# Performance work log

Measured on AMD Instinct MI355X. Metric: run time of the kernel, lower is better.

## Reference

```python
import jax, jax.numpy as jnp
import numpy as np
from jax import lax

EPS = 1e-5
NBIT = 127.0  # 8-bit symmetric: 2^(8-1)-1

def ste_round(x):
    return x + lax.stop_gradient(jnp.round(x) - x)

def quant_act(x, rng_max):
    # symmetric fake-quant of activations with learned per-cluster range
    s = rng_max / NBIT
    xq = jnp.clip(ste_round(x / s), -NBIT, NBIT) * s
    return xq, s

def fold_bn(w, gamma, beta, mean, var):
    std = jnp.sqrt(var + EPS)
    scale = gamma / std
    w_f = w * scale[:, None, None, None]
    b_f = beta - mean * scale
    return w_f, b_f

def quant_weight(w):
    # per-output-channel symmetric quant
    s = jnp.max(jnp.abs(w), axis=(1, 2, 3), keepdims=True) / NBIT
    wq = jnp.clip(ste_round(w / s), -NBIT, NBIT) * s
    return wq, s.reshape(-1)

def conv(x, w, stride=1, groups=1, pad=0):
    return lax.conv_general_dilated(
        x, w, window_strides=(stride, stride),
        padding=((pad, pad), (pad, pad)),
        dimension_numbers=('NCHW', 'OIHW', 'NCHW'),
        feature_group_count=groups)

def setup_inputs() -> dict:
    key = jax.random.key(0)
    ks = jax.random.split(key, 24)
    B, Cin, H, W = 64, 96, 28, 28
    Cmid, Cout, NC = 576, 96, 4
    d = {}
    d['x'] = jax.random.normal(ks[0], (B, Cin, H, W), dtype=jnp.float32)
    # conv1: 1x1 expansion
    d['w1'] = jax.random.normal(ks[1], (Cmid, Cin, 1, 1), jnp.float32) * 0.1
    d['g1'] = jax.random.uniform(ks[2], (Cmid,), minval=0.5, maxval=1.5)
    d['b1'] = jax.random.normal(ks[3], (Cmid,)) * 0.1
    d['m1'] = jax.random.normal(ks[4], (Cmid,)) * 0.1
    d['v1'] = jax.random.uniform(ks[5], (Cmid,), minval=0.5, maxval=1.5)
    # conv2: 3x3 depthwise
    d['w2'] = jax.random.normal(ks[6], (Cmid, 1, 3, 3), jnp.float32) * 0.1
    d['g2'] = jax.random.uniform(ks[7], (Cmid,), minval=0.5, maxval=1.5)
    d['b2'] = jax.random.normal(ks[8], (Cmid,)) * 0.1
    d['m2'] = jax.random.normal(ks[9], (Cmid,)) * 0.1
    d['v2'] = jax.random.uniform(ks[10], (Cmid,), minval=0.5, maxval=1.5)
    # conv3: 1x1 projection
    d['w3'] = jax.random.normal(ks[11], (Cout, Cmid, 1, 1), jnp.float32) * 0.1
    d['g3'] = jax.random.uniform(ks[12], (Cout,), minval=0.5, maxval=1.5)
    d['b3'] = jax.random.normal(ks[13], (Cout,)) * 0.1
    d['m3'] = jax.random.normal(ks[14], (Cout,)) * 0.1
    d['v3'] = jax.random.uniform(ks[15], (Cout,), minval=0.5, maxval=1.5)
    # per-cluster learned activation ranges for the 4 QuantAct modules
    d['r0'] = jax.random.uniform(ks[16], (NC,), minval=2.0, maxval=8.0)
    d['r1'] = jax.random.uniform(ks[17], (NC,), minval=2.0, maxval=8.0)
    d['r2'] = jax.random.uniform(ks[18], (NC,), minval=2.0, maxval=8.0)
    d['r3'] = jax.random.uniform(ks[19], (NC,), minval=2.0, maxval=8.0)
    d['cluster'] = 2
    return d

def reference(x, w1, g1, b1, m1, v1, w2, g2, b2, m2, v2,
              w3, g3, b3, m3, v3, r0, r1, r2, r3, cluster):
    identity = x  # residual path (in==out, stride==1)
    # QuantAct -> conv1 (BN-folded, per-channel quant) -> ReLU6
    xq, s0 = quant_act(x, r0[cluster])
    w1f, bf1 = fold_bn(w1, g1, b1, m1, v1)
    w1q, ws1 = quant_weight(w1f)
    y = conv(xq, w1q) + bf1[None, :, None, None]
    y = jnp.clip(y, 0.0, 6.0)
    # QuantAct1 -> depthwise conv2 -> ReLU6
    yq, s1 = quant_act(y, r1[cluster])
    w2f, bf2 = fold_bn(w2, g2, b2, m2, v2)
    w2q, ws2 = quant_weight(w2f)
    y = conv(yq, w2q, stride=1, groups=w2.shape[0], pad=1) + bf2[None, :, None, None]
    y = jnp.clip(y, 0.0, 6.0)
    # QuantAct2 -> conv3 projection
    yq, s2 = quant_act(y, r2[cluster])
    w3f, bf3 = fold_bn(w3, g3, b3, m3, v3)
    w3q, ws3 = quant_weight(w3f)
    y = conv(yq, w3q) + bf3[None, :, None, None]
    # residual add, then int32 requant
    y = y + identity
    out, s3 = quant_act(y, r3[cluster])
    return out, s3
```

## Files before the change

### kernel.cpp

```cpp
#include <hip/hip_runtime.h>
#include <cstdint>
#include <cstddef>

typedef int   v4i __attribute__((ext_vector_type(4)));
typedef float v4f __attribute__((ext_vector_type(4)));
typedef unsigned int u32;

constexpr int B_   = 64;
constexpr int CIN  = 96;
constexpr int P_   = 784;
constexpr int CMID = 576;
constexpr int COUT = 96;
constexpr int NOUT = B_ * COUT * P_;
constexpr float NBITF = 127.0f;
constexpr float EPSF  = 1e-5f;
constexpr float MAGICF = 12582912.0f;
constexpr int   BIASI  = 0x4B400000;

constexpr int Y1S = 43;

__device__ __forceinline__ int dot3(u32 a, u32 w, int acc) {
#if __has_builtin(__builtin_amdgcn_sdot4)
    return __builtin_amdgcn_sdot4((int)a, (int)w, acc, false);
#else
    return acc + (int)(signed char)(a)        * (int)(signed char)(w)
               + (int)(signed char)(a >> 8)   * (int)(signed char)(w >> 8)
               + (int)(signed char)(a >> 16)  * (int)(signed char)(w >> 16);
#endif
}

__device__ __forceinline__ void tr4(u32 S0, u32 S1, u32 S2, u32 S3, u32 O[4]) {
    u32 u01 = __builtin_amdgcn_perm(S1, S0, 0x05010400u);
    u32 u23 = __builtin_amdgcn_perm(S3, S2, 0x05010400u);
    u32 v01 = __builtin_amdgcn_perm(S1, S0, 0x07030602u);
    u32 v23 = __builtin_amdgcn_perm(S3, S2, 0x07030602u);
    O[0] = __builtin_amdgcn_perm(u23, u01, 0x05040100u);
    O[1] = __builtin_amdgcn_perm(u23, u01, 0x07060302u);
    O[2] = __builtin_amdgcn_perm(v23, v01, 0x05040100u);
    O[3] = __builtin_amdgcn_perm(v23, v01, 0x07060302u);
}

__device__ __forceinline__ u32 pack4(u32 t0, u32 t1, u32 t2, u32 t3) {
    u32 p01 = __builtin_amdgcn_perm(t1, t0, 0x05010400u);
    u32 p23 = __builtin_amdgcn_perm(t3, t2, 0x05010400u);
    return __builtin_amdgcn_perm(p23, p01, 0x05040100u);
}

__global__ __launch_bounds__(256)
void prep_w(const float* __restrict__ w1, const float* __restrict__ g1,
            const float* __restrict__ b1, const float* __restrict__ m1,
            const float* __restrict__ v1,
            const float* __restrict__ w2, const float* __restrict__ g2,
            const float* __restrict__ b2, const float* __restrict__ m2,
            const float* __restrict__ v2,
            const float* __restrict__ w3, const float* __restrict__ g3,
            const float* __restrict__ b3, const float* __restrict__ m3,
            const float* __restrict__ v3,
            const float* __restrict__ r0, const float* __restrict__ r1,
            const float* __restrict__ r2, const int* __restrict__ cluster,
            int8_t* __restrict__ w1qp, float2* __restrict__ e1,
            v4i* __restrict__ w2pk,    float2* __restrict__ e2,
            int8_t* __restrict__ w3qp, float2* __restrict__ e3)
{
    int tid = threadIdx.x;
    int c = cluster[0];
    int lane = tid & 63, wv = tid >> 6;
    int blk = blockIdx.x * 4 + wv;

    const float *w, *g, *bb, *mm, *vv;
    int oc, K, which;
    if (blk < CMID)            { which = 0; w = w1; g = g1; bb = b1; mm = m1; vv = v1; oc = blk;            K = CIN;  }
    else if (blk < 2 * CMID)   { which = 1; w = w2; g = g2; bb = b2; mm = m2; vv = v2; oc = blk - CMID;     K = 9;    }
    else                       { which = 2; w = w3; g = g3; bb = b3; mm = m3; vv = v3; oc = blk - 2 * CMID; K = CMID; }

    float scale = g[oc] / sqrtf(vv[oc] + EPSF);

    float mx = 0.f;
    for (int k = lane; k < K; k += 64)
        mx = fmaxf(mx, fabsf(w[oc * K + k] * scale));
    #pragma unroll
    for (int off = 1; off < 64; off <<= 1)
        mx = fmaxf(mx, __shfl_xor(mx, off));

    float s = mx / NBITF;

    int myq = 0;
    for (int k = lane; k < K; k += 64) {
        float wf = w[oc * K + k] * scale;
        float q  = fminf(fmaxf(rintf(wf / s), -127.f), 127.f);
        if (which == 0)      w1qp[oc * 144 + k] = (int8_t)q;
        else if (which == 1) myq = (int)q;
        else                 w3qp[oc * 592 + k] = (int8_t)q;
    }
    if (which == 0 && lane < 12)
        ((u32*)(w1qp + oc * 144))[24 + lane] = 0u;
    if (which == 1) {
        u32 qq[9];
        #pragma unroll
        for (int t = 0; t < 9; t++) qq[t] = (u32)__shfl(myq, t, 64) & 0xffu;
        if (lane == 0) {
            v4i pk;
            pk[0] = (int)(qq[0] | (qq[1] << 8) | (qq[2] << 16));
            pk[1] = (int)(qq[3] | (qq[4] << 8) | (qq[5] << 16));
            pk[2] = (int)(qq[6] | (qq[7] << 8) | (qq[8] << 16));
            pk[3] = 0;
            w2pk[oc] = pk;
        }
    }
    if (lane == 0) {
        float bf = bb[oc] - mm[oc] * scale;
        float s0 = r0[c] / NBITF, s1 = r1[c] / NBITF, s2 = r2[c] / NBITF;
        if (which == 0) {
            float inv_s1 = NBITF / r1[c];
            e1[oc] = make_float2(s0 * s * inv_s1, bf * inv_s1);
        } else if (which == 1) {
            float inv_s2 = NBITF / r2[c];
            e2[oc] = make_float2(s1 * s * inv_s2, bf * inv_s2);
        } else {
            e3[oc] = make_float2(s2 * s, bf);
        }
    }
}

__global__ __launch_bounds__(256, 2)
void conv123d(const v4i* __restrict__ w1q4,
              const float2* __restrict__ e1,
              const v4i* __restrict__ w2pk, const float2* __restrict__ e2,
              const int8_t* __restrict__ w3qp, const float2* __restrict__ e3,
              const float* __restrict__ x,
              const float* __restrict__ r0,
              const float* __restrict__ r1, const float* __restrict__ r2,
              const float* __restrict__ r3, const int* __restrict__ cluster,
              float* __restrict__ out)
{
    __shared__ v4i xw[11 * 6 * 16];
    __shared__ u32 y1s[4][48 * Y1S];
    __shared__ v4i y2c[12 * 112];

    int tid = threadIdx.x, b = blockIdx.y, rt = blockIdx.x;
    int R0 = 4 * rt;
    int W0 = (R0 - 1) * 28;
    int lane = tid & 63, wv = tid >> 6;
    int n = lane & 15, q4 = lane >> 4;

    int   c      = cluster[0];
    float inv_s0 = NBITF / r0[c];
    int   u1i    = (int)fminf(rintf(6.f * NBITF / r1[c]), 127.f);
    int   u2i    = (int)fminf(rintf(6.f * NBITF / r2[c]), 127.f);
    float s3     = r3[c] / NBITF;
    float inv_s3 = NBITF / r3[c];

    for (int i = tid; i < 4224; i += 256) {
        int nn = i & 15;
        int q  = (i >> 4) & 3;
        int gj = i >> 6;
        int g  = gj % 6, jm = gj / 6;
        int px = min(max(W0 + 16 * jm + nn, 0), P_ - 1);
        const float* xp = x + ((size_t)b * CIN + 16 * g + 4 * q) * P_ + px;
        int qv[4];
        #pragma unroll
        for (int j = 0; j < 4; j++) {
            float xf = xp[j * P_];
            qv[j] = (int)fminf(fmaxf(rintf(xf * inv_s0), -127.f), 127.f);
        }
        u32 t0 = __builtin_amdgcn_perm((u32)qv[1], (u32)qv[0], 0x00000400u);
        u32 t1 = __builtin_amdgcn_perm((u32)qv[3], (u32)qv[2], 0x00000400u);
        ((u32*)xw)[((jm * 6 + g) * 16 + nn) * 4 + q] =
            __builtin_amdgcn_perm(t1, t0, 0x05040100u);
    }

    u32* myY1 = y1s[wv];

    int pxl0 = wv * 32 + n;
    int pxc0 = min(pxl0, 111);
    int pxc1 = min(pxl0 + 16, 111);
    int sx0  = 28 * (pxc0 & 3) + (pxc0 >> 2);
    int sx1  = 28 * (pxc1 & 3) + (pxc1 >> 2);
    const v4i* w34 = (const v4i*)w3qp;
    v4i acc3[2][6];
    #pragma unroll
    for (int h = 0; h < 2; h++)
        #pragma unroll
        for (int i = 0; i < 6; i++) acc3[h][i] = (v4i){0, 0, 0, 0};

    __syncthreads();

    for (int ph = 0; ph < 3; ph++) {
        int oc0 = ph * 192 + wv * 48;

        v4i    bw[3][2];
        float2 ee[3];
        #pragma unroll
        for (int jn = 0; jn < 3; jn++) {
            int oc = oc0 + 16 * jn + n;
            bw[jn][0] = w1q4[oc * 9 + q4];
            bw[jn][1] = w1q4[oc * 9 + 4 + q4];
            ee[jn] = e1[oc];
        }
        #pragma unroll
        for (int jm = 0; jm < 11; jm++) {
            v4i af0 = xw[(jm * 6 + q4) * 16 + n];
            v4i af1 = (q4 < 2) ? xw[(jm * 6 + 4 + q4) * 16 + n]
                               : (v4i){0, 0, 0, 0};
            int dw = 4 * jm + q4;
            bool inimg = (unsigned)(W0 + 4 * dw) < (unsigned)P_;

            #pragma unroll
            for (int jn = 0; jn < 3; jn++) {
                v4i acc = (v4i){0, 0, 0, 0};
                acc = __builtin_amdgcn_mfma_i32_16x16x64_i8(af0, bw[jn][0], acc, 0, 0, 0);
                acc = __builtin_amdgcn_mfma_i32_16x16x64_i8(af1, bw[jn][1], acc, 0, 0, 0);
                u32 t[4];
                #pragma unroll
                for (int r = 0; r < 4; r++) {
                    float f = fmaf((float)acc[r], ee[jn].x, ee[jn].y) + MAGICF;
                    t[r] = (u32)min(max(__float_as_int(f), BIASI), BIASI + u1i);
                }
                u32 pk = pack4(t[0], t[1], t[2], t[3]);
                if (dw < 42)
                    myY1[(16 * jn + n) * Y1S + dw] = inimg ? pk : 0u;
            }
        }

        #pragma unroll
        for (int p = 0; p < 3; p++) {
            int id   = p * 64 + lane;
            int chl  = id >> 2;
            int orow = id & 3;
            int ch   = oc0 + chl;
            int rb   = chl * Y1S + orow * 7;

            v4i wpk = w2pk[ch];
            u32 pk0 = (u32)wpk[0], pk1 = (u32)wpk[1], pk2 = (u32)wpk[2];
            float2 e = e2[ch];

            u32 W[3][7];
            #pragma unroll
            for (int r = 0; r < 3; r++)
                #pragma unroll
                for (int w = 0; w < 7; w++)
                    W[r][w] = myY1[rb + r * 7 + w];

            __builtin_amdgcn_sched_barrier(0);

            u32 outw[7];
            #pragma unroll
            for (int xq = 0; xq < 7; xq++) {
                u32 M0 = xq ? W[0][xq - 1] : 0u;
                u32 M1 = xq ? W[1][xq - 1] : 0u;
                u32 M2 = xq ? W[2][xq - 1] : 0u;
                u32 D0 = W[0][xq], D1 = W[1][xq], D2 = W[2][xq];
                u32 N0 = (xq < 6) ? W[0][xq + 1] : 0u;
                u32 N1 = (xq < 6) ? W[1][xq + 1] : 0u;
                u32 N2 = (xq < 6) ? W[2][xq + 1] : 0u;

                int a0, a1, a2, a3;
                a0 = dot3(__builtin_amdgcn_alignbyte(D0, M0, 3), pk0, 0);
                a0 = dot3(__builtin_amdgcn_alignbyte(D1, M1, 3), pk1, a0);
                a0 = dot3(__builtin_amdgcn_alignbyte(D2, M2, 3), pk2, a0);
                a1 = dot3(D0, pk0, 0);
                a1 = dot3(D1, pk1, a1);
                a1 = dot3(D2, pk2, a1);
                a2 = dot3(__builtin_amdgcn_alignbyte(N0, D0, 1), pk0, 0);
                a2 = dot3(__builtin_amdgcn_alignbyte(N1, D1, 1), pk1, a2);
                a2 = dot3(__builtin_amdgcn_alignbyte(N2, D2, 1), pk2, a2);
                a3 = dot3(__builtin_amdgcn_alignbyte(N0, D0, 2), pk0, 0);
                a3 = dot3(__builtin_amdgcn_alignbyte(N1, D1, 2), pk1, a3);
                a3 = dot3(__builtin_amdgcn_alignbyte(N2, D2, 2), pk2, a3);

                int aa[4] = {a0, a1, a2, a3};
                u32 tq[4];
                #pragma unroll
                for (int i = 0; i < 4; i++) {
                    float f = fmaf((float)aa[i], e.x, e.y) + MAGICF;
                    tq[i] = (u32)min(max(__float_as_int(f), BIASI), BIASI + u2i);
                }
                outw[xq] = pack4(tq[0], tq[1], tq[2], tq[3]);
            }

            #pragma unroll
            for (int xq = 0; xq < 7; xq++)
                myY1[chl * Y1S + orow * 7 + xq] = outw[xq];
        }

        for (int u = lane; u < 84; u += 64) {
            int kgl = u / 28, d = u - kgl * 28;
            u32 O[4][4];
            #pragma unroll
            for (int j = 0; j < 4; j++) {
                int ch0 = 16 * kgl + 4 * j;
                tr4(myY1[(ch0 + 0) * Y1S + d], myY1[(ch0 + 1) * Y1S + d],
                    myY1[(ch0 + 2) * Y1S + d], myY1[(ch0 + 3) * Y1S + d], O[j]);
            }
            int kgG = wv * 3 + kgl;
            #pragma unroll
            for (int i = 0; i < 4; i++)
                y2c[kgG * 112 + 28 * i + d] =
                    (v4i){(int)O[0][i], (int)O[1][i], (int)O[2][i], (int)O[3][i]};
        }

        __syncthreads();

        #pragma unroll
        for (int ks = 0; ks < 3; ks++) {
            v4i bfr0 = y2c[(4 * ks + q4) * 112 + sx0];
            v4i bfr1 = y2c[(4 * ks + q4) * 112 + sx1];
            #pragma unroll
            for (int i = 0; i < 6; i++) {
                v4i afr = w34[(i * 16 + n) * 37 + ph * 12 + 4 * ks + q4];
                acc3[0][i] = __builtin_amdgcn_mfma_i32_16x16x64_i8(afr, bfr0, acc3[0][i], 0, 0, 0);
                acc3[1][i] = __builtin_amdgcn_mfma_i32_16x16x64_i8(afr, bfr1, acc3[1][i], 0, 0, 0);
            }
        }

        if (ph < 2) __syncthreads();
    }

    #pragma unroll
    for (int h = 0; h < 2; h++) {
        int pxl = pxl0 + 16 * h;
        if (pxl < 112) {
            int px = R0 * 28 + pxl;
            #pragma unroll
            for (int i = 0; i < 6; i++) {
                #pragma unroll
                for (int r = 0; r < 4; r++) {
                    int    oc = i * 16 + q4 * 4 + r;
                    float2 e  = e3[oc];
                    size_t gi = (size_t)(b * COUT + oc) * P_ + px;
                    float v  = fmaf((float)acc3[h][i][r], e.x, e.y) + x[gi];
                    float f  = fmaf(v, inv_s3, MAGICF);
                    int lvl  = min(max(__float_as_int(f) - BIASI, -127), 127);
                    out[gi]  = (float)lvl * s3;
                }
            }
        }
    }
    if (rt == 0 && b == 0 && tid == 0)
        out[NOUT] = s3;
}

extern "C" void kernel_launch(void* const* d_in, const int* in_sizes, int n_in,
                              void* d_out, int out_size, void* d_ws, size_t ws_size,
                              hipStream_t stream)
{
    const float* x  = (const float*)d_in[0];
    const float* w1 = (const float*)d_in[1];
    const float* g1 = (const float*)d_in[2];
    const float* b1 = (const float*)d_in[3];
    const float* m1 = (const float*)d_in[4];
    const float* v1 = (const float*)d_in[5];
    const float* w2 = (const float*)d_in[6];
    const float* g2 = (const float*)d_in[7];
    const float* b2 = (const float*)d_in[8];
    const float* m2 = (const float*)d_in[9];
    const float* v2 = (const float*)d_in[10];
    const float* w3 = (const float*)d_in[11];
    const float* g3 = (const float*)d_in[12];
    const float* b3 = (const float*)d_in[13];
    const float* m3 = (const float*)d_in[14];
    const float* v3 = (const float*)d_in[15];
    const float* r0 = (const float*)d_in[16];
    const float* r1 = (const float*)d_in[17];
    const float* r2 = (const float*)d_in[18];
    const float* r3 = (const float*)d_in[19];
    const int*   cl = (const int*)d_in[20];

    float* out = (float*)d_out;

    char*  ws  = (char*)d_ws;
    size_t off = 0;
    auto carve = [&](size_t bytes) {
        size_t cur = off;
        off = (off + bytes + 255) & ~(size_t)255;
        return (void*)(ws + cur);
    };
    int8_t* w1qp = (int8_t*)carve((size_t)CMID * 144);
    float2* e1   = (float2*)carve((size_t)CMID * 8);
    v4i*    w2pk = (v4i*)carve((size_t)CMID * 16);
    float2* e2   = (float2*)carve((size_t)CMID * 8);
    int8_t* w3qp = (int8_t*)carve((size_t)COUT * 592);
    float2* e3   = (float2*)carve((size_t)COUT * 8);
    (void)ws_size; (void)in_sizes; (void)n_in; (void)out_size;

    prep_w<<<dim3(312), dim3(256), 0, stream>>>(
        w1, g1, b1, m1, v1, w2, g2, b2, m2, v2, w3, g3, b3, m3, v3,
        r0, r1, r2, cl,
        w1qp, e1, w2pk, e2, w3qp, e3);

    conv123d<<<dim3(7, B_), dim3(256), 0, stream>>>(
        (const v4i*)w1qp, e1, w2pk, e2, w3qp, e3,
        x, r0, r1, r2, r3, cl, out);
}
```

Before: 154.7 us.

## Reuse per-wave y1 LDS slice for transposed conv3 operands, raise occupancy to 3

Drops the separate y2c shared buffer and writes the transposed int8 conv3 operands back into each wave's own y1s slice, which cuts LDS per block. The conv3 MFMA B-fragment reads are re-indexed into those slices. Launch bounds go from 2 to 3 blocks per CU so the freed LDS can host more resident blocks. The transpose loop is unrolled into two predicated passes with sched barriers so every read of a slice finishes before that slice is overwritten. The risks are register pressure under the tighter launch bound and a possible read/write hazard inside the slice.

```diff
diff --git a/kernel.cpp b/kernel.cpp
--- a/kernel.cpp
+++ b/kernel.cpp
@@ -17,7 +17,9 @@
 constexpr float MAGICF = 12582912.0f;
 constexpr int   BIASI  = 0x4B400000;
 
-constexpr int Y1S = 43;
+constexpr int Y1S  = 43;
+constexpr int YWW  = 48 * Y1S;
+constexpr int YWV4 = YWW / 4;
 
 __device__ __forceinline__ int dot3(u32 a, u32 w, int acc) {
 #if __has_builtin(__builtin_amdgcn_sdot4)
@@ -122,7 +124,7 @@
     }
 }
 
-__global__ __launch_bounds__(256, 2)
+__global__ __launch_bounds__(256, 3)
 void conv123d(const v4i* __restrict__ w1q4,
               const float2* __restrict__ e1,
               const v4i* __restrict__ w2pk, const float2* __restrict__ e2,
@@ -134,8 +136,7 @@
               float* __restrict__ out)
 {
     __shared__ v4i xw[11 * 6 * 16];
-    __shared__ u32 y1s[4][48 * Y1S];
-    __shared__ v4i y2c[12 * 112];
+    __shared__ __align__(16) u32 y1s[4][YWW];
 
     int tid = threadIdx.x, b = blockIdx.y, rt = blockIdx.x;
     int R0 = 4 * rt;
@@ -176,6 +177,13 @@
     int pxc1 = min(pxl0 + 16, 111);
     int sx0  = 28 * (pxc0 & 3) + (pxc0 >> 2);
     int sx1  = 28 * (pxc1 & 3) + (pxc1 >> 2);
+    int sb[3];
+    #pragma unroll
+    for (int ks = 0; ks < 3; ks++) {
+        int kg = 4 * ks + q4;
+        sb[ks] = (kg / 3) * YWV4 + (kg % 3) * 112;
+    }
+    const v4i* y1v = (const v4i*)y1s;
     const v4i* w34 = (const v4i*)w3qp;
     v4i acc3[2][6];
     #pragma unroll
@@ -283,8 +291,13 @@
                 myY1[chl * Y1S + orow * 7 + xq] = outw[xq];
         }
 
-        for (int u = lane; u < 84; u += 64) {
-            int kgl = u / 28, d = u - kgl * 28;
+        v4i* slice = (v4i*)y1s[wv];
+        #pragma unroll
+        for (int pass = 0; pass < 2; pass++) {
+            int u   = pass * 64 + lane;
+            bool act = u < 84;
+            int uu  = min(u, 83);
+            int kgl = uu / 28, d = uu - kgl * 28;
             u32 O[4][4];
             #pragma unroll
             for (int j = 0; j < 4; j++) {
@@ -292,19 +305,22 @@
                 tr4(myY1[(ch0 + 0) * Y1S + d], myY1[(ch0 + 1) * Y1S + d],
                     myY1[(ch0 + 2) * Y1S + d], myY1[(ch0 + 3) * Y1S + d], O[j]);
             }
-            int kgG = wv * 3 + kgl;
-            #pragma unroll
-            for (int i = 0; i < 4; i++)
-                y2c[kgG * 112 + 28 * i + d] =
-                    (v4i){(int)O[0][i], (int)O[1][i], (int)O[2][i], (int)O[3][i]};
+            __builtin_amdgcn_sched_barrier(0);
+            if (act) {
+                #pragma unroll
+                for (int i = 0; i < 4; i++)
+                    slice[kgl * 112 + 28 * i + d] =
+                        (v4i){(int)O[0][i], (int)O[1][i], (int)O[2][i], (int)O[3][i]};
+            }
+            __builtin_amdgcn_sched_barrier(0);
         }
 
         __syncthreads();
 
         #pragma unroll
         for (int ks = 0; ks < 3; ks++) {
-            v4i bfr0 = y2c[(4 * ks + q4) * 112 + sx0];
-            v4i bfr1 = y2c[(4 * ks + q4) * 112 + sx1];
+            v4i bfr0 = y1v[sb[ks] + sx0];
+            v4i bfr1 = y1v[sb[ks] + sx1];
             #pragma unroll
             for (int i = 0; i < 6; i++) {
                 v4i afr = w34[(i * 16 + n) * 37 + ph * 12 + 4 * ks + q4];
```

Result: no change. 155.2 us (+0.3%).
